# Kernel optimization log

Measured on AMD Instinct MI355X. Metric: run time of the kernel, lower is better.

## Reference

```python
import jax, jax.numpy as jnp
import numpy as np

T, H, E = 1024, 2048, 32
I = 1024            # moe_intermediate_size
K = 8               # num_experts_per_token
G = 4               # num_expert_group
TOPK_GROUP = 2
N_SHARED = 2
IS = I * N_SHARED   # shared-expert intermediate
RSF = 2.5           # routed_scaling_factor


def setup_inputs() -> dict:
    key = jax.random.key(0)
    ks = jax.random.split(key, 9)
    s = 0.02
    return {
        "hidden_states": jax.random.normal(ks[0], (T, H), jnp.float32),
        "gate_w": jax.random.normal(ks[1], (H, E), jnp.float32) * s,
        "corr_bias": jax.random.normal(ks[2], (E,), jnp.float32) * s,
        "w_gate": jax.random.normal(ks[3], (E, H, I), jnp.float32) * s,
        "w_up": jax.random.normal(ks[4], (E, H, I), jnp.float32) * s,
        "w_down": jax.random.normal(ks[5], (E, I, H), jnp.float32) * s,
        "sw_gate": jax.random.normal(ks[6], (H, IS), jnp.float32) * s,
        "sw_up": jax.random.normal(ks[7], (H, IS), jnp.float32) * s,
        "sw_down": jax.random.normal(ks[8], (IS, H), jnp.float32) * s,
    }


def _route(x, gate_w, corr_bias):
    # biased grouped top-k (DeepSeek-V3 style sigmoid routing)
    logits = x @ gate_w                      # [T,E]
    scores = jax.nn.sigmoid(logits)
    sfc = scores + corr_bias[None, :]        # scores for choice
    grp = sfc.reshape(-1, G, E // G)
    # group score = sum of top-2 biased scores within the group
    grp_score = jax.lax.top_k(grp, 2)[0].sum(-1)          # [T,G]
    _, gidx = jax.lax.top_k(grp_score, TOPK_GROUP)        # [T,topk_group]
    rows = jnp.arange(sfc.shape[0])[:, None]
    gmask = jnp.zeros((sfc.shape[0], G), sfc.dtype).at[rows, gidx].set(1.0)
    emask = jnp.repeat(gmask, E // G, axis=1)             # [T,E]
    masked = jnp.where(emask > 0, sfc, -jnp.inf)
    _, idx = jax.lax.top_k(masked, K)                     # [T,K]
    w = jnp.take_along_axis(scores, idx, axis=1)          # unbiased scores
    w = w / w.sum(-1, keepdims=True)                      # renormalize
    w = w * RSF                                           # routed scaling
    combine = jnp.zeros((sfc.shape[0], E), x.dtype).at[rows, idx].add(w)
    return combine                                        # dense [T,E] combine weights


def reference(hidden_states, gate_w, corr_bias, w_gate, w_up, w_down,
              sw_gate, sw_up, sw_down):
    x = hidden_states
    # shared experts (SiLU-gated MLP)
    shared = (jax.nn.silu(x @ sw_gate) * (x @ sw_up)) @ sw_down   # [T,H]
    # routing
    combine = _route(x, gate_w, corr_bias)                        # [T,E]
    # routed experts (dense grouped-GEMM reference)
    g = jnp.einsum('th,ehi->tei', x, w_gate)
    u = jnp.einsum('th,ehi->tei', x, w_up)
    a = jax.nn.silu(g) * u                                        # [T,E,I]
    y = jnp.einsum('tei,eih->teh', a, w_down)                     # [T,E,H]
    routed = jnp.einsum('teh,te->th', y, combine)
    return routed + shared
```

## Files before the change

### kernel.cpp

```cpp
#include <hip/hip_runtime.h>

#define T_TOK 1024
#define H_DIM 2048
#define E_NUM 32
#define I_DIM 1024
#define IS_DIM 2048

typedef float  f32x4 __attribute__((ext_vector_type(4)));
typedef short  s16x8 __attribute__((ext_vector_type(8)));
typedef unsigned short u16x4 __attribute__((ext_vector_type(4)));
typedef unsigned short u16x8 __attribute__((ext_vector_type(8)));

__device__ __forceinline__ unsigned short f2bf(float f) {
    unsigned u = __builtin_bit_cast(unsigned, f);
    u = (u + 0x7fffu + ((u >> 16) & 1u)) >> 16;
    return (unsigned short)u;
}

__device__ __forceinline__ int swz(int r, int c) {
    return (r << 5) + (c ^ (((r >> 2) & 3) << 3));
}

__global__ __launch_bounds__(256) void cvt_k(
    const float* __restrict__ x, unsigned short* __restrict__ xb)
{
    const int i = (blockIdx.x * 256 + threadIdx.x) * 8;
    f32x4 a = *(const f32x4*)(x + i);
    f32x4 b = *(const f32x4*)(x + i + 4);
    u16x8 h = { f2bf(a[0]), f2bf(a[1]), f2bf(a[2]), f2bf(a[3]),
                f2bf(b[0]), f2bf(b[1]), f2bf(b[2]), f2bf(b[3]) };
    *(u16x8*)(xb + i) = h;
}

__global__ __launch_bounds__(256) void route_k(
    const float* __restrict__ x, const float* __restrict__ gw,
    const float* __restrict__ bias, int* __restrict__ tidx,
    float* __restrict__ tw)
{
    const int w = threadIdx.x >> 6;
    const int lane = threadIdx.x & 63;
    const int t = blockIdx.x * 4 + w;
    __shared__ float xs[4][H_DIM];
    __shared__ float sfc[4][E_NUM];
    __shared__ float sc[4][E_NUM];

    for (int i = threadIdx.x; i < 4 * (H_DIM / 4); i += 256) {
        int tt = i >> 9;
        int c = i & 511;
        *(f32x4*)&xs[tt][c * 4] =
            *(const f32x4*)(x + (size_t)(blockIdx.x * 4 + tt) * H_DIM + c * 4);
    }
    __syncthreads();

    const int eq = (lane & 7) * 4;
    const int hs = lane >> 3;
    f32x4 acc = {0.f, 0.f, 0.f, 0.f};
    #pragma unroll 4
    for (int h = hs; h < H_DIM; h += 8) {
        float xv = xs[w][h];
        f32x4 gv = *(const f32x4*)(gw + (size_t)h * E_NUM + eq);
        acc += gv * xv;
    }
    #pragma unroll
    for (int m = 8; m < 64; m <<= 1) {
        acc[0] += __shfl_xor(acc[0], m);
        acc[1] += __shfl_xor(acc[1], m);
        acc[2] += __shfl_xor(acc[2], m);
        acc[3] += __shfl_xor(acc[3], m);
    }
    if (lane < 8) {
        #pragma unroll
        for (int j = 0; j < 4; ++j) {
            float s = 1.f / (1.f + expf(-acc[j]));
            sc[w][eq + j] = s;
            sfc[w][eq + j] = s + bias[eq + j];
        }
    }
    __syncthreads();

    if (lane == 0) {
        float gs[4];
        for (int gg = 0; gg < 4; ++gg) {
            float m1 = -1e30f, m2 = -1e30f;
            for (int j = 0; j < 8; ++j) {
                float v = sfc[w][gg * 8 + j];
                if (v > m1) { m2 = m1; m1 = v; }
                else if (v > m2) { m2 = v; }
            }
            gs[gg] = m1 + m2;
        }
        int g1 = 0;
        for (int gg = 1; gg < 4; ++gg) if (gs[gg] > gs[g1]) g1 = gg;
        int g2 = (g1 == 0) ? 1 : 0;
        for (int gg = 0; gg < 4; ++gg)
            if (gg != g1 && gs[gg] > gs[g2]) g2 = gg;

        unsigned allow = (0xFFu << (g1 * 8)) | (0xFFu << (g2 * 8));
        unsigned taken = 0u;
        int   isel[8];
        float wsel[8];
        float wsum = 0.f;
        for (int k = 0; k < 8; ++k) {
            int best = 0; float bv = -1e30f;
            for (int e2 = 0; e2 < 32; ++e2) {
                if (((allow >> e2) & 1u) && !((taken >> e2) & 1u)) {
                    float v = sfc[w][e2];
                    if (v > bv) { bv = v; best = e2; }
                }
            }
            taken |= 1u << best;
            isel[k] = best;
            wsel[k] = sc[w][best];
            wsum += sc[w][best];
        }
        const float f = 2.5f / wsum;
        for (int k = 0; k < 8; ++k) {
            tidx[t * 8 + k] = isel[k];
            tw[t * 8 + k] = wsel[k] * f;
        }
    }
}

__global__ __launch_bounds__(64) void build_k(
    const int* __restrict__ tidx, const float* __restrict__ tw,
    int* __restrict__ ltok, float* __restrict__ lw, int* __restrict__ counts)
{
    const int e = blockIdx.x;
    const int lane = threadIdx.x;
    int cnt = 0;
    for (int t0 = 0; t0 < T_TOK; t0 += 64) {
        const int t = t0 + lane;
        int sel = 0; float w = 0.f;
        #pragma unroll
        for (int k = 0; k < 8; ++k) {
            if (tidx[t * 8 + k] == e) { sel = 1; w = tw[t * 8 + k]; }
        }
        unsigned long long m = __ballot(sel);
        int pos = __popcll(m & ((1ull << lane) - 1ull));
        if (sel) {
            ltok[e * T_TOK + cnt + pos] = t;
            lw[e * T_TOK + cnt + pos] = w;
        }
        cnt += __popcll(m);
    }
    if (lane == 0) counts[e] = cnt;
}

__global__ void prefix_k(const int* __restrict__ counts, int* __restrict__ offsets)
{
    if (threadIdx.x == 0) {
        int off = 0;
        for (int e = 0; e < E_NUM; ++e) { offsets[e] = off; off += counts[e]; }
    }
}

template<int DUAL, int EXPERT, int GATHER, int ATOMIC, int BM>
__global__ __launch_bounds__(256, 4) void gemm_k(
    const unsigned short* __restrict__ A, const float* __restrict__ B1g,
    const float* __restrict__ B2g, void* __restrict__ outv,
    const int* __restrict__ counts, const int* __restrict__ offsets,
    const int* __restrict__ ltok, const float* __restrict__ lw,
    int M, int N, int K)
{
    constexpr int WR  = BM / 2;
    constexpr int FM  = WR / 16;
    constexpr int TPR = 256 / BM;
    constexpr int KSP = 32 / TPR;
    constexpr int NB  = KSP / 8;

    const int e = blockIdx.z;
    const int Mloc = EXPERT ? counts[e] : M;
    const int col0 = blockIdx.y * 64;
    const int rb = EXPERT ? offsets[e] : 0;

    const float* B1 = B1g;
    const float* B2 = B2g;
    if (EXPERT) {
        size_t eo = (size_t)e * K * N;
        B1 += eo;
        if (DUAL) B2 += eo;
    }

    __shared__ unsigned short lA[2][BM * 32];
    __shared__ unsigned short lB[2][DUAL + 1][64 * 32];

    const int tid = threadIdx.x;
    const int lane = tid & 63;
    const int wv = tid >> 6;
    const int wm = wv >> 1;
    const int wn = wv & 1;

    const int arow = tid / TPR;
    const int akb  = (tid % TPR) * KSP;

    const bool doB = tid < (DUAL ? 256 : 128);
    const int bmat = DUAL ? (tid >> 7) : 0;
    const int t7 = tid & 127;
    const int nq = t7 & 15;
    const int kq = t7 >> 4;
    const float* bp = (bmat ? B2 : B1) + (size_t)(4 * kq) * N + col0 + nq * 4;

    f32x4 acc1[FM][2], acc2[FM][2];
    u16x8 pbaX[NB], pbaY[NB];
    f32x4 pbX[4], pbY[4];
    const unsigned short* apb = nullptr;

    auto loadT = [&](int k0, u16x8 (&pba)[NB], f32x4 (&pb)[4]) {
        #pragma unroll
        for (int i = 0; i < NB; ++i)
            pba[i] = *(const u16x8*)(apb + k0 + i * 8);
        if (doB) {
            #pragma unroll
            for (int j = 0; j < 4; ++j)
                pb[j] = *(const f32x4*)(bp + (size_t)(k0 + j) * N);
        }
    };

    auto storeT = [&](int p, u16x8 (&pba)[NB], f32x4 (&pb)[4]) {
        #pragma unroll
        for (int i = 0; i < NB; ++i)
            *(u16x8*)&lA[p][swz(arow, akb + i * 8)] = pba[i];
        if (doB) {
            #pragma unroll
            for (int j2 = 0; j2 < 4; ++j2) {
                u16x4 h = { f2bf(pb[0][j2]), f2bf(pb[1][j2]),
                            f2bf(pb[2][j2]), f2bf(pb[3][j2]) };
                *(u16x4*)&lB[p][bmat][swz(nq * 4 + j2, kq * 4)] = h;
            }
        }
    };

    auto compute = [&](int p) {
        const int koff = (lane >> 4) * 8;
        s16x8 af[FM], b1f[2], b2f[2];
        #pragma unroll
        for (int fm = 0; fm < FM; ++fm)
            af[fm] = *(const s16x8*)&lA[p][swz(wm * WR + fm * 16 + (lane & 15), koff)];
        #pragma unroll
        for (int fn = 0; fn < 2; ++fn) {
            b1f[fn] = *(const s16x8*)&lB[p][0][swz(wn * 32 + fn * 16 + (lane & 15), koff)];
            if (DUAL)
                b2f[fn] = *(const s16x8*)&lB[p][1][swz(wn * 32 + fn * 16 + (lane & 15), koff)];
        }
        #pragma unroll
        for (int fm = 0; fm < FM; ++fm)
            #pragma unroll
            for (int fn = 0; fn < 2; ++fn) {
                acc1[fm][fn] = __builtin_amdgcn_mfma_f32_16x16x32_bf16(
                    af[fm], b1f[fn], acc1[fm][fn], 0, 0, 0);
                if (DUAL)
                    acc2[fm][fn] = __builtin_amdgcn_mfma_f32_16x16x32_bf16(
                        af[fm], b2f[fn], acc2[fm][fn], 0, 0, 0);
            }
    };

    const int nk = K >> 5;

    for (int row0 = blockIdx.x * BM; row0 < Mloc; row0 += gridDim.x * BM) {
        {
            int rr = row0 + arow;
            if (rr >= Mloc) rr = Mloc - 1;
            int grow = GATHER ? ltok[e * T_TOK + rr] : (rb + rr);
            apb = A + (size_t)grow * K + akb;
        }
        #pragma unroll
        for (int a = 0; a < FM; ++a)
            #pragma unroll
            for (int b = 0; b < 2; ++b) {
                acc1[a][b] = f32x4{0.f, 0.f, 0.f, 0.f};
                acc2[a][b] = f32x4{0.f, 0.f, 0.f, 0.f};
            }

        loadT(0, pbaX, pbX);
        loadT(32, pbaY, pbY);
        __syncthreads();
        storeT(0, pbaX, pbX);
        __syncthreads();

        for (int kt = 0; kt < nk; kt += 2) {
            if (kt + 2 < nk) loadT((kt + 2) << 5, pbaX, pbX);
            compute(0);
            storeT(1, pbaY, pbY);
            __syncthreads();
            if (kt + 3 < nk) loadT((kt + 3) << 5, pbaY, pbY);
            compute(1);
            if (kt + 2 < nk) {
                storeT(0, pbaX, pbX);
                __syncthreads();
            }
        }

        const int fr = (lane >> 4) << 2;
        const int fc = lane & 15;
        if (DUAL) {
            unsigned short* outp = (unsigned short*)outv;
            #pragma unroll
            for (int fm = 0; fm < FM; ++fm)
                #pragma unroll
                for (int fn = 0; fn < 2; ++fn)
                    #pragma unroll
                    for (int j = 0; j < 4; ++j) {
                        int r = wm * WR + fm * 16 + fr + j;
                        if (row0 + r < Mloc) {
                            int cc = col0 + wn * 32 + fn * 16 + fc;
                            float gv = acc1[fm][fn][j];
                            float uv = acc2[fm][fn][j];
                            float a = gv / (1.f + expf(-gv)) * uv;
                            outp[(size_t)(rb + row0 + r) * N + cc] = f2bf(a);
                        }
                    }
        } else if (ATOMIC) {
            float* outp = (float*)outv;
            #pragma unroll
            for (int fm = 0; fm < FM; ++fm)
                #pragma unroll
                for (int fn = 0; fn < 2; ++fn)
                    #pragma unroll
                    for (int j = 0; j < 4; ++j) {
                        int r = wm * WR + fm * 16 + fr + j;
                        if (row0 + r < Mloc) {
                            int tok = ltok[e * T_TOK + row0 + r];
                            float wr = lw[e * T_TOK + row0 + r];
                            int cc = col0 + wn * 32 + fn * 16 + fc;
                            atomicAdd(outp + (size_t)tok * N + cc, acc1[fm][fn][j] * wr);
                        }
                    }
        } else {
            float* outp = (float*)outv;
            #pragma unroll
            for (int fm = 0; fm < FM; ++fm)
                #pragma unroll
                for (int fn = 0; fn < 2; ++fn)
                    #pragma unroll
                    for (int j = 0; j < 4; ++j) {
                        int r = wm * WR + fm * 16 + fr + j;
                        if (row0 + r < Mloc) {
                            int cc = col0 + wn * 32 + fn * 16 + fc;
                            outp[(size_t)(row0 + r) * N + cc] = acc1[fm][fn][j];
                        }
                    }
        }
    }
}

extern "C" void kernel_launch(void* const* d_in, const int* in_sizes, int n_in,
                              void* d_out, int out_size, void* d_ws, size_t ws_size,
                              hipStream_t stream) {
    const float* x       = (const float*)d_in[0];
    const float* gate_w  = (const float*)d_in[1];
    const float* bias    = (const float*)d_in[2];
    const float* w_gate  = (const float*)d_in[3];
    const float* w_up    = (const float*)d_in[4];
    const float* w_down  = (const float*)d_in[5];
    const float* sw_gate = (const float*)d_in[6];
    const float* sw_up   = (const float*)d_in[7];
    const float* sw_down = (const float*)d_in[8];
    float* out = (float*)d_out;

    char* ws = (char*)d_ws;
    int*   topk_idx = (int*)ws;
    float* topk_w   = (float*)(ws + 32768);
    int*   counts   = (int*)(ws + 65536);
    int*   offsets  = (int*)(ws + 65536 + 128);
    int*   ltok     = (int*)(ws + 65536 + 256);
    float* lw       = (float*)(ws + 65536 + 256 + 131072);
    unsigned short* act_s = (unsigned short*)(ws + 65536 + 256 + 262144);
    unsigned short* act_r = act_s + (size_t)T_TOK * IS_DIM;
    unsigned short* xbf   = act_r + (size_t)T_TOK * 8 * I_DIM;

    cvt_k<<<T_TOK * H_DIM / 2048, 256, 0, stream>>>(x, xbf);
    route_k<<<T_TOK / 4, 256, 0, stream>>>(x, gate_w, bias, topk_idx, topk_w);
    build_k<<<E_NUM, 64, 0, stream>>>(topk_idx, topk_w, ltok, lw, counts);
    prefix_k<<<1, 64, 0, stream>>>(counts, offsets);

    gemm_k<1,0,0,0,64><<<dim3(16, 32, 1), 256, 0, stream>>>(
        xbf, sw_gate, sw_up, act_s, nullptr, nullptr, nullptr, nullptr,
        T_TOK, IS_DIM, H_DIM);
    gemm_k<1,1,1,0,128><<<dim3(2, 16, 32), 256, 0, stream>>>(
        xbf, w_gate, w_up, act_r, counts, offsets, ltok, lw,
        T_TOK, I_DIM, H_DIM);
    gemm_k<0,0,0,0,64><<<dim3(16, 32, 1), 256, 0, stream>>>(
        act_s, sw_down, nullptr, out, nullptr, nullptr, nullptr, nullptr,
        T_TOK, H_DIM, IS_DIM);
    gemm_k<0,1,0,1,128><<<dim3(2, 32, 32), 256, 0, stream>>>(
        act_r, w_down, nullptr, out, counts, offsets, ltok, lw,
        T_TOK, H_DIM, I_DIM);
}
```

Measured before the change: 855.7 us.

## Use 128x32 block tiles with four row-stacked waves for all GEMMs

Replaces the templated BM tile (64 or 128 rows by 64 columns, 2x2 wave grid) with a fixed 128x32 tile where each of the four waves owns 32 rows and the full 32 columns. The B (fp32 weight) load now covers only 32 columns per block, so fewer threads convert weights, and grids are reshaped to one row-block per expert with twice as many column blocks. The goal is to cut redundant weight reads and conversion per block and to give the expert GEMMs more parallel blocks. The cost is lower arithmetic intensity per A tile, since A is re-read for every 32-column slice, and the launch-bounds occupancy hint is removed.

```diff
diff --git a/kernel.cpp b/kernel.cpp
--- a/kernel.cpp
+++ b/kernel.cpp
@@ -154,23 +154,22 @@
     }
 }
 
-template<int DUAL, int EXPERT, int GATHER, int ATOMIC, int BM>
-__global__ __launch_bounds__(256, 4) void gemm_k(
+template<int DUAL, int EXPERT, int GATHER, int ATOMIC>
+__global__ __launch_bounds__(256) void gemm_k(
     const unsigned short* __restrict__ A, const float* __restrict__ B1g,
     const float* __restrict__ B2g, void* __restrict__ outv,
     const int* __restrict__ counts, const int* __restrict__ offsets,
     const int* __restrict__ ltok, const float* __restrict__ lw,
     int M, int N, int K)
 {
-    constexpr int WR  = BM / 2;
-    constexpr int FM  = WR / 16;
-    constexpr int TPR = 256 / BM;
-    constexpr int KSP = 32 / TPR;
-    constexpr int NB  = KSP / 8;
+    constexpr int BM = 128;
+    constexpr int WR = 32;
+    constexpr int FM = 2;
+    constexpr int NB = 2;
 
     const int e = blockIdx.z;
     const int Mloc = EXPERT ? counts[e] : M;
-    const int col0 = blockIdx.y * 64;
+    const int col0 = blockIdx.y * 32;
     const int rb = EXPERT ? offsets[e] : 0;
 
     const float* B1 = B1g;
@@ -182,22 +181,20 @@
     }
 
     __shared__ unsigned short lA[2][BM * 32];
-    __shared__ unsigned short lB[2][DUAL + 1][64 * 32];
+    __shared__ unsigned short lB[2][DUAL + 1][32 * 32];
 
     const int tid = threadIdx.x;
     const int lane = tid & 63;
     const int wv = tid >> 6;
-    const int wm = wv >> 1;
-    const int wn = wv & 1;
-
-    const int arow = tid / TPR;
-    const int akb  = (tid % TPR) * KSP;
-
-    const bool doB = tid < (DUAL ? 256 : 128);
-    const int bmat = DUAL ? (tid >> 7) : 0;
-    const int t7 = tid & 127;
-    const int nq = t7 & 15;
-    const int kq = t7 >> 4;
+
+    const int arow = tid >> 1;
+    const int akb  = (tid & 1) * 16;
+
+    const bool doB = tid < (DUAL ? 128 : 64);
+    const int bmat = DUAL ? (tid >> 6) : 0;
+    const int t6 = tid & 63;
+    const int nq = t6 & 7;
+    const int kq = t6 >> 3;
     const float* bp = (bmat ? B2 : B1) + (size_t)(4 * kq) * N + col0 + nq * 4;
 
     f32x4 acc1[FM][2], acc2[FM][2];
@@ -235,12 +232,12 @@
         s16x8 af[FM], b1f[2], b2f[2];
         #pragma unroll
         for (int fm = 0; fm < FM; ++fm)
-            af[fm] = *(const s16x8*)&lA[p][swz(wm * WR + fm * 16 + (lane & 15), koff)];
+            af[fm] = *(const s16x8*)&lA[p][swz(wv * WR + fm * 16 + (lane & 15), koff)];
         #pragma unroll
         for (int fn = 0; fn < 2; ++fn) {
-            b1f[fn] = *(const s16x8*)&lB[p][0][swz(wn * 32 + fn * 16 + (lane & 15), koff)];
+            b1f[fn] = *(const s16x8*)&lB[p][0][swz(fn * 16 + (lane & 15), koff)];
             if (DUAL)
-                b2f[fn] = *(const s16x8*)&lB[p][1][swz(wn * 32 + fn * 16 + (lane & 15), koff)];
+                b2f[fn] = *(const s16x8*)&lB[p][1][swz(fn * 16 + (lane & 15), koff)];
         }
         #pragma unroll
         for (int fm = 0; fm < FM; ++fm)
@@ -300,9 +297,9 @@
                 for (int fn = 0; fn < 2; ++fn)
                     #pragma unroll
                     for (int j = 0; j < 4; ++j) {
-                        int r = wm * WR + fm * 16 + fr + j;
+                        int r = wv * WR + fm * 16 + fr + j;
                         if (row0 + r < Mloc) {
-                            int cc = col0 + wn * 32 + fn * 16 + fc;
+                            int cc = col0 + fn * 16 + fc;
                             float gv = acc1[fm][fn][j];
                             float uv = acc2[fm][fn][j];
                             float a = gv / (1.f + expf(-gv)) * uv;
@@ -317,11 +314,11 @@
                 for (int fn = 0; fn < 2; ++fn)
                     #pragma unroll
                     for (int j = 0; j < 4; ++j) {
-                        int r = wm * WR + fm * 16 + fr + j;
+                        int r = wv * WR + fm * 16 + fr + j;
                         if (row0 + r < Mloc) {
                             int tok = ltok[e * T_TOK + row0 + r];
                             float wr = lw[e * T_TOK + row0 + r];
-                            int cc = col0 + wn * 32 + fn * 16 + fc;
+                            int cc = col0 + fn * 16 + fc;
                             atomicAdd(outp + (size_t)tok * N + cc, acc1[fm][fn][j] * wr);
                         }
                     }
@@ -333,9 +330,9 @@
                 for (int fn = 0; fn < 2; ++fn)
                     #pragma unroll
                     for (int j = 0; j < 4; ++j) {
-                        int r = wm * WR + fm * 16 + fr + j;
+                        int r = wv * WR + fm * 16 + fr + j;
                         if (row0 + r < Mloc) {
-                            int cc = col0 + wn * 32 + fn * 16 + fc;
+                            int cc = col0 + fn * 16 + fc;
                             outp[(size_t)(row0 + r) * N + cc] = acc1[fm][fn][j];
                         }
                     }
@@ -373,16 +370,16 @@
     build_k<<<E_NUM, 64, 0, stream>>>(topk_idx, topk_w, ltok, lw, counts);
     prefix_k<<<1, 64, 0, stream>>>(counts, offsets);
 
-    gemm_k<1,0,0,0,64><<<dim3(16, 32, 1), 256, 0, stream>>>(
+    gemm_k<1,0,0,0><<<dim3(8, IS_DIM / 32, 1), 256, 0, stream>>>(
         xbf, sw_gate, sw_up, act_s, nullptr, nullptr, nullptr, nullptr,
         T_TOK, IS_DIM, H_DIM);
-    gemm_k<1,1,1,0,128><<<dim3(2, 16, 32), 256, 0, stream>>>(
+    gemm_k<1,1,1,0><<<dim3(1, I_DIM / 32, E_NUM), 256, 0, stream>>>(
         xbf, w_gate, w_up, act_r, counts, offsets, ltok, lw,
         T_TOK, I_DIM, H_DIM);
-    gemm_k<0,0,0,0,64><<<dim3(16, 32, 1), 256, 0, stream>>>(
+    gemm_k<0,0,0,0><<<dim3(8, H_DIM / 32, 1), 256, 0, stream>>>(
         act_s, sw_down, nullptr, out, nullptr, nullptr, nullptr, nullptr,
         T_TOK, H_DIM, IS_DIM);
-    gemm_k<0,1,0,1,128><<<dim3(2, 32, 32), 256, 0, stream>>>(
+    gemm_k<0,1,0,1><<<dim3(1, H_DIM / 32, E_NUM), 256, 0, stream>>>(
         act_r, w_down, nullptr, out, counts, offsets, ltok, lw,
         T_TOK, H_DIM, I_DIM);
 }
```

Result: faster. 783.2 us (-8.5%).
